# Performance work log

Measured on AMD Instinct MI355X. Metric: run time of the kernel, lower is better.

The kernel has to match this reference:

```python
import jax, jax.numpy as jnp
import numpy as np

HID, VOCAB, LAYERS, MAXLEN, SPAN = 1024, 32000, 4, 128, 2


def setup_inputs() -> dict:
    key = jax.random.key(0)
    ks = jax.random.split(key, 12)
    s = 0.02
    return {
        "input_ids": jax.random.randint(ks[0], (SPAN,), 0, VOCAB),
        "hidden": jax.random.normal(ks[1], (LAYERS, 1, HID), jnp.float32),
        "encoder_outputs": jax.random.normal(ks[2], (MAXLEN, HID), jnp.float32),
        "embedding": jax.random.normal(ks[3], (VOCAB, HID), jnp.float32) * s,
        "attn_W": jax.random.normal(ks[4], (MAXLEN, HID * (1 + SPAN)), jnp.float32) * s,
        "attn_b": jnp.zeros((MAXLEN,), jnp.float32),
        "comb_W": jax.random.normal(ks[5], (HID, HID * (1 + SPAN)), jnp.float32) * s,
        "comb_b": jnp.zeros((HID,), jnp.float32),
        "gru_Wih": jax.random.normal(ks[6], (LAYERS, 3 * HID, HID), jnp.float32) * s,
        "gru_Whh": jax.random.normal(ks[7], (LAYERS, 3 * HID, HID), jnp.float32) * s,
        "gru_bih": jnp.zeros((LAYERS, 3 * HID), jnp.float32),
        "gru_bhh": jnp.zeros((LAYERS, 3 * HID), jnp.float32),
        "out_W": jax.random.normal(ks[8], (VOCAB * SPAN, HID), jnp.float32) * s,
        "out_b": jnp.zeros((VOCAB * SPAN,), jnp.float32),
    }


def reference(input_ids, hidden, encoder_outputs, embedding, attn_W, attn_b,
              comb_W, comb_b, gru_Wih, gru_Whh, gru_bih, gru_bhh, out_W, out_b):
    # embed span tokens -> [1, SPAN*HID] (dropout = identity at eval)
    emb = embedding[input_ids].reshape(1, SPAN * HID)
    # attention over encoder outputs
    attn_in = jnp.concatenate([emb, hidden[0]], axis=1)          # [1, (1+SPAN)*HID]
    attn_weights = jax.nn.softmax(attn_in @ attn_W.T + attn_b, axis=1)  # [1, MAXLEN]
    attn_applied = attn_weights @ encoder_outputs                 # [1, HID]
    # combine + relu -> GRU input
    x = jax.nn.relu(jnp.concatenate([emb, attn_applied], axis=1) @ comb_W.T + comb_b)  # [1, HID]
    # multi-layer GRU single step (PyTorch gate order: r, z, n)
    new_h = []
    inp = x
    for l in range(LAYERS):
        h = hidden[l]                                             # [1, HID]
        gi = inp @ gru_Wih[l].T + gru_bih[l]                      # [1, 3*HID]
        gh = h @ gru_Whh[l].T + gru_bhh[l]
        i_r, i_z, i_n = jnp.split(gi, 3, axis=1)
        h_r, h_z, h_n = jnp.split(gh, 3, axis=1)
        r = jax.nn.sigmoid(i_r + h_r)
        z = jax.nn.sigmoid(i_z + h_z)
        n = jnp.tanh(i_n + r * h_n)
        h2 = (1.0 - z) * n + z * h
        new_h.append(h2)
        inp = h2
    hidden_new = jnp.stack(new_h)                                 # [LAYERS, 1, HID]
    # output projection, split into SPAN vocab chunks, log_softmax each
    logits = inp @ out_W.T + out_b                                # [1, SPAN*VOCAB]
    logp = jax.nn.log_softmax(logits.reshape(SPAN, VOCAB), axis=-1)  # [SPAN, VOCAB]
    return logp, hidden_new, attn_weights
```

## Files before the change

kernel.cpp:

```cpp
#include <hip/hip_runtime.h>
#include <math.h>

#define HID 1024
#define VOCAB 32000
#define LAYERS 4
#define MAXLEN 128
#define SPAN 2

#define OUT_LOGP 0
#define OUT_HID 64000
#define OUT_ATTNW 68096

#define WS_XCAT 0
#define WS_SCORES 3072
#define WS_X 3200
#define WS_RED 4224
#define WS_LOGITS 8192

__global__ __launch_bounds__(256) void k_scores(const int* __restrict__ ids,
                                                const float* __restrict__ hidden,
                                                const float* __restrict__ embedding,
                                                const float* __restrict__ attn_W,
                                                const float* __restrict__ attn_b,
                                                float* __restrict__ ws) {
    int b = blockIdx.x;
    int t = threadIdx.x;
    if (b < MAXLEN) {
        const float4* W4 = (const float4*)(attn_W + (size_t)b * 3072);
        float sum = 0.f;
#pragma unroll
        for (int i = 0; i < 3; i++) {
            int k4 = t + 256 * i;
            float4 w = W4[k4];
            int e = k4 * 4;
            float4 x;
            if (e < 2048) {
                int row = ids[e >> 10];
                x = *(const float4*)(embedding + (size_t)row * HID + (e & 1023));
            } else {
                x = *(const float4*)(hidden + (e - 2048));
            }
            sum += w.x * x.x + w.y * x.y + w.z * x.z + w.w * x.w;
        }
        __shared__ float sred[4];
        int lane = t & 63, wid = t >> 6;
        for (int o = 32; o > 0; o >>= 1) sum += __shfl_down(sum, o, 64);
        if (lane == 0) sred[wid] = sum;
        __syncthreads();
        if (t == 0) {
            float v = sred[0] + sred[1] + sred[2] + sred[3];
            ws[WS_SCORES + b] = v + attn_b[b];
        }
    } else {
        int idx = (b - MAXLEN) * 256 + t;
        int row = ids[idx >> 10];
        ws[WS_XCAT + idx] = embedding[(size_t)row * HID + (idx & 1023)];
    }
}

__global__ __launch_bounds__(128) void k_softmax_apply(const float* __restrict__ enc,
                                                       float* __restrict__ ws,
                                                       float* __restrict__ out) {
    __shared__ float w[MAXLEN];
    __shared__ float red[2];
    int t = threadIdx.x;
    int lane = t & 63, wid = t >> 6;
    float s = ws[WS_SCORES + t];
    float m = s;
    for (int o = 32; o > 0; o >>= 1) m = fmaxf(m, __shfl_down(m, o, 64));
    if (lane == 0) red[wid] = m;
    __syncthreads();
    float gmax = fmaxf(red[0], red[1]);
    __syncthreads();
    float e = expf(s - gmax);
    float sum = e;
    for (int o = 32; o > 0; o >>= 1) sum += __shfl_down(sum, o, 64);
    if (lane == 0) red[wid] = sum;
    __syncthreads();
    float gsum = red[0] + red[1];
    float wt = e / gsum;
    w[t] = wt;
    if (blockIdx.x == 0) out[OUT_ATTNW + t] = wt;
    __syncthreads();
    int i = blockIdx.x * 128 + t;
    float acc = 0.f;
#pragma unroll 16
    for (int k = 0; k < MAXLEN; k++) acc += w[k] * enc[(size_t)k * HID + i];
    ws[WS_XCAT + 2048 + i] = acc;
}

__global__ __launch_bounds__(256) void k_comb(const float* __restrict__ comb_W,
                                              const float* __restrict__ comb_b,
                                              float* __restrict__ ws) {
    int r = blockIdx.x, t = threadIdx.x;
    const float4* W4 = (const float4*)(comb_W + (size_t)r * 3072);
    const float4* x4 = (const float4*)(ws + WS_XCAT);
    float sum = 0.f;
#pragma unroll
    for (int i = 0; i < 3; i++) {
        int k4 = t + 256 * i;
        float4 w = W4[k4];
        float4 x = x4[k4];
        sum += w.x * x.x + w.y * x.y + w.z * x.z + w.w * x.w;
    }
    __shared__ float sred[4];
    int lane = t & 63, wid = t >> 6;
    for (int o = 32; o > 0; o >>= 1) sum += __shfl_down(sum, o, 64);
    if (lane == 0) sred[wid] = sum;
    __syncthreads();
    if (t == 0) {
        float v = sred[0] + sred[1] + sred[2] + sred[3];
        ws[WS_X + r] = fmaxf(v + comb_b[r], 0.f);
    }
}

__global__ __launch_bounds__(384) void k_gru(const float* __restrict__ inp,
                                             const float* __restrict__ h,
                                             const float* __restrict__ Wih,
                                             const float* __restrict__ Whh,
                                             const float* __restrict__ bih,
                                             const float* __restrict__ bhh,
                                             float* __restrict__ h_out) {
    int j = blockIdx.x;
    int t = threadIdx.x;
    int wv = t >> 6, lane = t & 63;
    __shared__ float dots[6];
    const float* W;
    const float* x;
    if (wv < 3) { W = Wih + ((size_t)wv * HID + j) * HID; x = inp; }
    else        { W = Whh + ((size_t)(wv - 3) * HID + j) * HID; x = h; }
    const float4* W4 = (const float4*)W;
    const float4* x4 = (const float4*)x;
    float sum = 0.f;
#pragma unroll
    for (int i = 0; i < 4; i++) {
        float4 w = W4[lane + 64 * i];
        float4 xx = x4[lane + 64 * i];
        sum += w.x * xx.x + w.y * xx.y + w.z * xx.z + w.w * xx.w;
    }
    for (int o = 32; o > 0; o >>= 1) sum += __shfl_down(sum, o, 64);
    if (lane == 0) dots[wv] = sum;
    __syncthreads();
    if (t == 0) {
        float ir = dots[0] + bih[j];
        float iz = dots[1] + bih[HID + j];
        float in_ = dots[2] + bih[2 * HID + j];
        float hr = dots[3] + bhh[j];
        float hz = dots[4] + bhh[HID + j];
        float hn = dots[5] + bhh[2 * HID + j];
        float rg = 1.f / (1.f + expf(-(ir + hr)));
        float zg = 1.f / (1.f + expf(-(iz + hz)));
        float ng = tanhf(in_ + rg * hn);
        h_out[j] = (1.f - zg) * ng + zg * h[j];
    }
}

__global__ __launch_bounds__(256) void k_logits(const float* __restrict__ h3,
                                                const float* __restrict__ out_W,
                                                const float* __restrict__ out_b,
                                                float* __restrict__ ws) {
    int wv = threadIdx.x >> 6, lane = threadIdx.x & 63;
    int r0 = (blockIdx.x * 4 + wv) * 4;
    const float4* x4 = (const float4*)h3;
    float4 xv[4];
#pragma unroll
    for (int i = 0; i < 4; i++) xv[i] = x4[lane + 64 * i];
    const float4* W4 = (const float4*)(out_W + (size_t)r0 * HID);
    float s[4] = {0.f, 0.f, 0.f, 0.f};
#pragma unroll
    for (int r = 0; r < 4; r++) {
#pragma unroll
        for (int i = 0; i < 4; i++) {
            float4 w = W4[r * 256 + lane + 64 * i];
            s[r] += w.x * xv[i].x + w.y * xv[i].y + w.z * xv[i].z + w.w * xv[i].w;
        }
    }
#pragma unroll
    for (int r = 0; r < 4; r++)
        for (int o = 32; o > 0; o >>= 1) s[r] += __shfl_down(s[r], o, 64);
    if (lane == 0) {
        float4 b = *(const float4*)(out_b + r0);
        float4 res = make_float4(s[0] + b.x, s[1] + b.y, s[2] + b.z, s[3] + b.w);
        *(float4*)(ws + WS_LOGITS + r0) = res;
    }
}

__global__ __launch_bounds__(256) void k_red(float* __restrict__ ws) {
    int b = blockIdx.x, t = threadIdx.x;
    int span = b >> 5, chunk = b & 31;
    int lane = t & 63, wid = t >> 6;
    const float* l = ws + WS_LOGITS + (size_t)span * VOCAB + chunk * 1000;
    __shared__ float sred[4];
    float m = -INFINITY;
    for (int i = t; i < 1000; i += 256) m = fmaxf(m, l[i]);
    for (int o = 32; o > 0; o >>= 1) m = fmaxf(m, __shfl_down(m, o, 64));
    if (lane == 0) sred[wid] = m;
    __syncthreads();
    float gmax = fmaxf(fmaxf(sred[0], sred[1]), fmaxf(sred[2], sred[3]));
    __syncthreads();
    float sum = 0.f;
    for (int i = t; i < 1000; i += 256) sum += expf(l[i] - gmax);
    for (int o = 32; o > 0; o >>= 1) sum += __shfl_down(sum, o, 64);
    if (lane == 0) sred[wid] = sum;
    __syncthreads();
    if (t == 0) {
        ws[WS_RED + b * 2] = gmax;
        ws[WS_RED + b * 2 + 1] = sred[0] + sred[1] + sred[2] + sred[3];
    }
}

__global__ __launch_bounds__(256) void k_logp(const float* __restrict__ ws,
                                              float* __restrict__ out) {
    int t = threadIdx.x;
    int i = blockIdx.x * 256 + t;
    int span = blockIdx.x / 125;
    __shared__ float gm_s, ls_s;
    if (t < 64) {
        float m = -INFINITY, sm = 0.f;
        if (t < 32) {
            m = ws[WS_RED + (span * 32 + t) * 2];
            sm = ws[WS_RED + (span * 32 + t) * 2 + 1];
        }
        float gm = m;
        for (int o = 32; o > 0; o >>= 1) gm = fmaxf(gm, __shfl_down(gm, o, 64));
        gm = __shfl(gm, 0, 64);
        float e = sm * expf(m - gm);
        for (int o = 32; o > 0; o >>= 1) e += __shfl_down(e, o, 64);
        if (t == 0) { gm_s = gm; ls_s = logf(e); }
    }
    __syncthreads();
    out[OUT_LOGP + i] = ws[WS_LOGITS + i] - gm_s - ls_s;
}

extern "C" void kernel_launch(void* const* d_in, const int* in_sizes, int n_in,
                              void* d_out, int out_size, void* d_ws, size_t ws_size,
                              hipStream_t stream) {
    const int* ids = (const int*)d_in[0];
    const float* hidden = (const float*)d_in[1];
    const float* enc = (const float*)d_in[2];
    const float* embedding = (const float*)d_in[3];
    const float* attn_W = (const float*)d_in[4];
    const float* attn_b = (const float*)d_in[5];
    const float* comb_W = (const float*)d_in[6];
    const float* comb_b = (const float*)d_in[7];
    const float* gru_Wih = (const float*)d_in[8];
    const float* gru_Whh = (const float*)d_in[9];
    const float* gru_bih = (const float*)d_in[10];
    const float* gru_bhh = (const float*)d_in[11];
    const float* out_W = (const float*)d_in[12];
    const float* out_b = (const float*)d_in[13];
    float* out = (float*)d_out;
    float* ws = (float*)d_ws;

    k_scores<<<136, 256, 0, stream>>>(ids, hidden, embedding, attn_W, attn_b, ws);
    k_softmax_apply<<<8, 128, 0, stream>>>(enc, ws, out);
    k_comb<<<1024, 256, 0, stream>>>(comb_W, comb_b, ws);
    for (int l = 0; l < LAYERS; l++) {
        const float* inp = (l == 0) ? (ws + WS_X) : (out + OUT_HID + (l - 1) * HID);
        k_gru<<<1024, 384, 0, stream>>>(inp,
                                        hidden + (size_t)l * HID,
                                        gru_Wih + (size_t)l * 3 * HID * HID,
                                        gru_Whh + (size_t)l * 3 * HID * HID,
                                        gru_bih + (size_t)l * 3 * HID,
                                        gru_bhh + (size_t)l * 3 * HID,
                                        out + OUT_HID + l * HID);
    }
    k_logits<<<4000, 256, 0, stream>>>(out + OUT_HID + 3 * HID, out_W, out_b, ws);
    k_red<<<64, 256, 0, stream>>>(ws);
    k_logp<<<250, 256, 0, stream>>>(ws, out);
}
```

Measured before the change: 513.4 us.

## Hoist GRU hidden matvecs into first kernel and fuse softmax partials into logits

The Whh·h products for all four GRU layers depend only on the input hidden state, so they are computed up front in the first kernel alongside the attention scores. This takes the serial layer-to-layer chain down to just the Wih half and halves the threads per GRU block. The logits kernel now does 8 rows per wave and emits per-block online-softmax partials, which removes the separate reduction kernel; k_logp merges 1000 partials per span. The attention-apply kernel is also spread over more blocks, at the cost of a bigger first launch and extra workspace.

```diff
diff --git a/kernel.cpp b/kernel.cpp
--- a/kernel.cpp
+++ b/kernel.cpp
@@ -14,17 +14,25 @@
 #define WS_XCAT 0
 #define WS_SCORES 3072
 #define WS_X 3200
-#define WS_RED 4224
-#define WS_LOGITS 8192
-
-__global__ __launch_bounds__(256) void k_scores(const int* __restrict__ ids,
-                                                const float* __restrict__ hidden,
-                                                const float* __restrict__ embedding,
-                                                const float* __restrict__ attn_W,
-                                                const float* __restrict__ attn_b,
-                                                float* __restrict__ ws) {
+#define WS_GH 4224
+#define WS_RED 16512
+#define WS_LOGITS 24576
+
+__device__ __forceinline__ float dot4(float4 a, float4 b) {
+    return a.x * b.x + a.y * b.y + a.z * b.z + a.w * b.w;
+}
+
+__global__ __launch_bounds__(256) void k_pre(const int* __restrict__ ids,
+                                             const float* __restrict__ hidden,
+                                             const float* __restrict__ embedding,
+                                             const float* __restrict__ attn_W,
+                                             const float* __restrict__ attn_b,
+                                             const float* __restrict__ gru_Whh,
+                                             const float* __restrict__ gru_bhh,
+                                             float* __restrict__ ws) {
     int b = blockIdx.x;
     int t = threadIdx.x;
+    int lane = t & 63, wv = t >> 6;
     if (b < MAXLEN) {
         const float4* W4 = (const float4*)(attn_W + (size_t)b * 3072);
         float sum = 0.f;
@@ -40,53 +48,70 @@
             } else {
                 x = *(const float4*)(hidden + (e - 2048));
             }
-            sum += w.x * x.x + w.y * x.y + w.z * x.z + w.w * x.w;
+            sum += dot4(w, x);
         }
         __shared__ float sred[4];
-        int lane = t & 63, wid = t >> 6;
         for (int o = 32; o > 0; o >>= 1) sum += __shfl_down(sum, o, 64);
-        if (lane == 0) sred[wid] = sum;
+        if (lane == 0) sred[wv] = sum;
         __syncthreads();
         if (t == 0) {
             float v = sred[0] + sred[1] + sred[2] + sred[3];
             ws[WS_SCORES + b] = v + attn_b[b];
         }
-    } else {
+    } else if (b < MAXLEN + 8) {
         int idx = (b - MAXLEN) * 256 + t;
         int row = ids[idx >> 10];
         ws[WS_XCAT + idx] = embedding[(size_t)row * HID + (idx & 1023)];
-    }
-}
-
-__global__ __launch_bounds__(128) void k_softmax_apply(const float* __restrict__ enc,
+    } else {
+        int r = (b - MAXLEN - 8) * 4 + wv;
+        int l = r / 3072;
+        int g = r - l * 3072;
+        const float4* W4 = (const float4*)(gru_Whh + ((size_t)l * 3072 + g) * HID);
+        const float4* h4 = (const float4*)(hidden + (size_t)l * HID);
+        float sum = 0.f;
+#pragma unroll
+        for (int i = 0; i < 4; i++) {
+            int k4 = lane + 64 * i;
+            sum += dot4(W4[k4], h4[k4]);
+        }
+        for (int o = 32; o > 0; o >>= 1) sum += __shfl_down(sum, o, 64);
+        if (lane == 0) ws[WS_GH + r] = sum + gru_bhh[r];
+    }
+}
+
+__global__ __launch_bounds__(256) void k_softmax_apply(const float* __restrict__ enc,
                                                        float* __restrict__ ws,
                                                        float* __restrict__ out) {
-    __shared__ float w[MAXLEN];
-    __shared__ float red[2];
+    __shared__ float w2[MAXLEN];
+    __shared__ float part[8][32];
     int t = threadIdx.x;
-    int lane = t & 63, wid = t >> 6;
-    float s = ws[WS_SCORES + t];
-    float m = s;
-    for (int o = 32; o > 0; o >>= 1) m = fmaxf(m, __shfl_down(m, o, 64));
-    if (lane == 0) red[wid] = m;
-    __syncthreads();
-    float gmax = fmaxf(red[0], red[1]);
-    __syncthreads();
-    float e = expf(s - gmax);
-    float sum = e;
-    for (int o = 32; o > 0; o >>= 1) sum += __shfl_down(sum, o, 64);
-    if (lane == 0) red[wid] = sum;
-    __syncthreads();
-    float gsum = red[0] + red[1];
-    float wt = e / gsum;
-    w[t] = wt;
-    if (blockIdx.x == 0) out[OUT_ATTNW + t] = wt;
-    __syncthreads();
-    int i = blockIdx.x * 128 + t;
-    float acc = 0.f;
-#pragma unroll 16
-    for (int k = 0; k < MAXLEN; k++) acc += w[k] * enc[(size_t)k * HID + i];
-    ws[WS_XCAT + 2048 + i] = acc;
+    if (t < 128) w2[t] = ws[WS_SCORES + t];
+    __syncthreads();
+    float m = -INFINITY;
+    for (int k = 0; k < 128; k++) m = fmaxf(m, w2[k]);
+    float s = 0.f;
+    for (int k = 0; k < 128; k++) s += expf(w2[k] - m);
+    __syncthreads();
+    if (t < 128) {
+        float wt = expf(w2[t] - m) / s;
+        if (blockIdx.x == 0) out[OUT_ATTNW + t] = wt;
+        w2[t] = wt;
+    }
+    __syncthreads();
+    int col = blockIdx.x * 32 + (t & 31);
+    int seg = t >> 5;
+    float p = 0.f;
+#pragma unroll
+    for (int k = 0; k < 16; k++)
+        p += w2[seg * 16 + k] * enc[(size_t)(seg * 16 + k) * HID + col];
+    part[seg][t & 31] = p;
+    __syncthreads();
+    if (t < 32) {
+        float acc = 0.f;
+#pragma unroll
+        for (int s2 = 0; s2 < 8; s2++) acc += part[s2][t];
+        ws[WS_XCAT + 2048 + blockIdx.x * 32 + t] = acc;
+    }
 }
 
 __global__ __launch_bounds__(256) void k_comb(const float* __restrict__ comb_W,
@@ -99,9 +124,7 @@
 #pragma unroll
     for (int i = 0; i < 3; i++) {
         int k4 = t + 256 * i;
-        float4 w = W4[k4];
-        float4 x = x4[k4];
-        sum += w.x * x.x + w.y * x.y + w.z * x.z + w.w * x.w;
+        sum += dot4(W4[k4], x4[k4]);
     }
     __shared__ float sred[4];
     int lane = t & 63, wid = t >> 6;
@@ -114,29 +137,23 @@
     }
 }
 
-__global__ __launch_bounds__(384) void k_gru(const float* __restrict__ inp,
+__global__ __launch_bounds__(192) void k_gru(const float* __restrict__ inp,
                                              const float* __restrict__ h,
                                              const float* __restrict__ Wih,
-                                             const float* __restrict__ Whh,
                                              const float* __restrict__ bih,
-                                             const float* __restrict__ bhh,
+                                             const float* __restrict__ gh,
                                              float* __restrict__ h_out) {
     int j = blockIdx.x;
     int t = threadIdx.x;
     int wv = t >> 6, lane = t & 63;
-    __shared__ float dots[6];
-    const float* W;
-    const float* x;
-    if (wv < 3) { W = Wih + ((size_t)wv * HID + j) * HID; x = inp; }
-    else        { W = Whh + ((size_t)(wv - 3) * HID + j) * HID; x = h; }
-    const float4* W4 = (const float4*)W;
-    const float4* x4 = (const float4*)x;
+    __shared__ float dots[3];
+    const float4* W4 = (const float4*)(Wih + ((size_t)wv * HID + j) * HID);
+    const float4* x4 = (const float4*)inp;
     float sum = 0.f;
 #pragma unroll
     for (int i = 0; i < 4; i++) {
-        float4 w = W4[lane + 64 * i];
-        float4 xx = x4[lane + 64 * i];
-        sum += w.x * xx.x + w.y * xx.y + w.z * xx.z + w.w * xx.w;
+        int k4 = lane + 64 * i;
+        sum += dot4(W4[k4], x4[k4]);
     }
     for (int o = 32; o > 0; o >>= 1) sum += __shfl_down(sum, o, 64);
     if (lane == 0) dots[wv] = sum;
@@ -145,9 +162,9 @@
         float ir = dots[0] + bih[j];
         float iz = dots[1] + bih[HID + j];
         float in_ = dots[2] + bih[2 * HID + j];
-        float hr = dots[3] + bhh[j];
-        float hz = dots[4] + bhh[HID + j];
-        float hn = dots[5] + bhh[2 * HID + j];
+        float hr = gh[j];
+        float hz = gh[HID + j];
+        float hn = gh[2 * HID + j];
         float rg = 1.f / (1.f + expf(-(ir + hr)));
         float zg = 1.f / (1.f + expf(-(iz + hz)));
         float ng = tanhf(in_ + rg * hn);
@@ -160,75 +177,94 @@
                                                 const float* __restrict__ out_b,
                                                 float* __restrict__ ws) {
     int wv = threadIdx.x >> 6, lane = threadIdx.x & 63;
-    int r0 = (blockIdx.x * 4 + wv) * 4;
+    int r0 = blockIdx.x * 32 + wv * 8;
     const float4* x4 = (const float4*)h3;
     float4 xv[4];
 #pragma unroll
     for (int i = 0; i < 4; i++) xv[i] = x4[lane + 64 * i];
     const float4* W4 = (const float4*)(out_W + (size_t)r0 * HID);
-    float s[4] = {0.f, 0.f, 0.f, 0.f};
-#pragma unroll
-    for (int r = 0; r < 4; r++) {
-#pragma unroll
-        for (int i = 0; i < 4; i++) {
-            float4 w = W4[r * 256 + lane + 64 * i];
-            s[r] += w.x * xv[i].x + w.y * xv[i].y + w.z * xv[i].z + w.w * xv[i].w;
-        }
-    }
-#pragma unroll
-    for (int r = 0; r < 4; r++)
+    float s[8];
+#pragma unroll
+    for (int r = 0; r < 8; r++) {
+        s[r] = 0.f;
+#pragma unroll
+        for (int k = 0; k < 4; k++)
+            s[r] += dot4(W4[r * 256 + lane + 64 * k], xv[k]);
+    }
+#pragma unroll
+    for (int r = 0; r < 8; r++)
         for (int o = 32; o > 0; o >>= 1) s[r] += __shfl_down(s[r], o, 64);
+    __shared__ float sm[4], ss[4];
     if (lane == 0) {
-        float4 b = *(const float4*)(out_b + r0);
-        float4 res = make_float4(s[0] + b.x, s[1] + b.y, s[2] + b.z, s[3] + b.w);
-        *(float4*)(ws + WS_LOGITS + r0) = res;
-    }
-}
-
-__global__ __launch_bounds__(256) void k_red(float* __restrict__ ws) {
-    int b = blockIdx.x, t = threadIdx.x;
-    int span = b >> 5, chunk = b & 31;
-    int lane = t & 63, wid = t >> 6;
-    const float* l = ws + WS_LOGITS + (size_t)span * VOCAB + chunk * 1000;
-    __shared__ float sred[4];
-    float m = -INFINITY;
-    for (int i = t; i < 1000; i += 256) m = fmaxf(m, l[i]);
-    for (int o = 32; o > 0; o >>= 1) m = fmaxf(m, __shfl_down(m, o, 64));
-    if (lane == 0) sred[wid] = m;
-    __syncthreads();
-    float gmax = fmaxf(fmaxf(sred[0], sred[1]), fmaxf(sred[2], sred[3]));
-    __syncthreads();
-    float sum = 0.f;
-    for (int i = t; i < 1000; i += 256) sum += expf(l[i] - gmax);
-    for (int o = 32; o > 0; o >>= 1) sum += __shfl_down(sum, o, 64);
-    if (lane == 0) sred[wid] = sum;
-    __syncthreads();
-    if (t == 0) {
-        ws[WS_RED + b * 2] = gmax;
-        ws[WS_RED + b * 2 + 1] = sred[0] + sred[1] + sred[2] + sred[3];
+        float4 b0 = *(const float4*)(out_b + r0);
+        float4 b1 = *(const float4*)(out_b + r0 + 4);
+        float v0 = s[0] + b0.x, v1 = s[1] + b0.y, v2 = s[2] + b0.z, v3 = s[3] + b0.w;
+        float v4 = s[4] + b1.x, v5 = s[5] + b1.y, v6 = s[6] + b1.z, v7 = s[7] + b1.w;
+        *(float4*)(ws + WS_LOGITS + r0) = make_float4(v0, v1, v2, v3);
+        *(float4*)(ws + WS_LOGITS + r0 + 4) = make_float4(v4, v5, v6, v7);
+        float vv[8] = {v0, v1, v2, v3, v4, v5, v6, v7};
+        float M = vv[0], S = 1.f;
+#pragma unroll
+        for (int r = 1; r < 8; r++) {
+            float v = vv[r];
+            if (v > M) { S = S * expf(M - v) + 1.f; M = v; }
+            else S += expf(v - M);
+        }
+        sm[wv] = M; ss[wv] = S;
+    }
+    __syncthreads();
+    if (threadIdx.x == 0) {
+        float M = sm[0], S = ss[0];
+#pragma unroll
+        for (int k = 1; k < 4; k++) {
+            float mk = sm[k], sk = ss[k];
+            if (mk > M) { S = S * expf(M - mk) + sk; M = mk; }
+            else S += sk * expf(mk - M);
+        }
+        ws[WS_RED + blockIdx.x * 2] = M;
+        ws[WS_RED + blockIdx.x * 2 + 1] = S;
     }
 }
 
 __global__ __launch_bounds__(256) void k_logp(const float* __restrict__ ws,
                                               float* __restrict__ out) {
-    int t = threadIdx.x;
-    int i = blockIdx.x * 256 + t;
-    int span = blockIdx.x / 125;
+    int t = threadIdx.x, b = blockIdx.x;
+    int span = b / 125;
+    int lane = t & 63, wv = t >> 6;
+    __shared__ float sm[4], ss[4];
     __shared__ float gm_s, ls_s;
-    if (t < 64) {
-        float m = -INFINITY, sm = 0.f;
-        if (t < 32) {
-            m = ws[WS_RED + (span * 32 + t) * 2];
-            sm = ws[WS_RED + (span * 32 + t) * 2 + 1];
-        }
-        float gm = m;
-        for (int o = 32; o > 0; o >>= 1) gm = fmaxf(gm, __shfl_down(gm, o, 64));
-        gm = __shfl(gm, 0, 64);
-        float e = sm * expf(m - gm);
-        for (int o = 32; o > 0; o >>= 1) e += __shfl_down(e, o, 64);
-        if (t == 0) { gm_s = gm; ls_s = logf(e); }
-    }
-    __syncthreads();
+    float M = -INFINITY, S = 0.f;
+#pragma unroll
+    for (int k = 0; k < 4; k++) {
+        int p = t + 256 * k;
+        if (p < 1000) {
+            float mk = ws[WS_RED + (span * 1000 + p) * 2];
+            float sk = ws[WS_RED + (span * 1000 + p) * 2 + 1];
+            if (mk > M) { S = S * expf(M - mk) + sk; M = mk; }
+            else S += sk * expf(mk - M);
+        }
+    }
+    for (int o = 32; o > 0; o >>= 1) {
+        float Mo = __shfl_down(M, o, 64);
+        float So = __shfl_down(S, o, 64);
+        float nM = fmaxf(M, Mo);
+        S = S * expf(M - nM) + So * expf(Mo - nM);
+        M = nM;
+    }
+    if (lane == 0) { sm[wv] = M; ss[wv] = S; }
+    __syncthreads();
+    if (t == 0) {
+        float Mf = sm[0], Sf = ss[0];
+#pragma unroll
+        for (int k = 1; k < 4; k++) {
+            float mk = sm[k], sk = ss[k];
+            if (mk > Mf) { Sf = Sf * expf(Mf - mk) + sk; Mf = mk; }
+            else Sf += sk * expf(mk - Mf);
+        }
+        gm_s = Mf; ls_s = logf(Sf);
+    }
+    __syncthreads();
+    int i = b * 256 + t;
     out[OUT_LOGP + i] = ws[WS_LOGITS + i] - gm_s - ls_s;
 }
 
@@ -252,20 +288,19 @@
     float* out = (float*)d_out;
     float* ws = (float*)d_ws;
 
-    k_scores<<<136, 256, 0, stream>>>(ids, hidden, embedding, attn_W, attn_b, ws);
-    k_softmax_apply<<<8, 128, 0, stream>>>(enc, ws, out);
+    k_pre<<<3208, 256, 0, stream>>>(ids, hidden, embedding, attn_W, attn_b,
+                                    gru_Whh, gru_bhh, ws);
+    k_softmax_apply<<<32, 256, 0, stream>>>(enc, ws, out);
     k_comb<<<1024, 256, 0, stream>>>(comb_W, comb_b, ws);
     for (int l = 0; l < LAYERS; l++) {
         const float* inp = (l == 0) ? (ws + WS_X) : (out + OUT_HID + (l - 1) * HID);
-        k_gru<<<1024, 384, 0, stream>>>(inp,
+        k_gru<<<1024, 192, 0, stream>>>(inp,
                                         hidden + (size_t)l * HID,
                                         gru_Wih + (size_t)l * 3 * HID * HID,
-                                        gru_Whh + (size_t)l * 3 * HID * HID,
                                         gru_bih + (size_t)l * 3 * HID,
-                                        gru_bhh + (size_t)l * 3 * HID,
+                                        ws + WS_GH + (size_t)l * 3 * HID,
                                         out + OUT_HID + l * HID);
     }
-    k_logits<<<4000, 256, 0, stream>>>(out + OUT_HID + 3 * HID, out_W, out_b, ws);
-    k_red<<<64, 256, 0, stream>>>(ws);
+    k_logits<<<2000, 256, 0, stream>>>(out + OUT_HID + 3 * HID, out_W, out_b, ws);
     k_logp<<<250, 256, 0, stream>>>(ws, out);
 }
```

New measurement: 511.1 us. No clear change (-0.5%).
